# Performance work log

Measured on AMD Instinct MI355X. Metric: run time of the kernel, lower is better.

Reference implementation:

```python
import jax, jax.numpy as jnp
import numpy as np

B, T, S, L = 1, 2048, 512, 1024
C, H, Hk, D = 2048, 16, 4, 128
THETA = 10000.0


def setup_inputs() -> dict:
    key = jax.random.key(0)
    ks = jax.random.split(key, 9)
    sd = 0.02
    return {
        "x": jax.random.normal(ks[0], (B, T, C), jnp.float32),
        "stm": jax.random.normal(ks[1], (B, S, C), jnp.float32),
        "long_q": jax.random.normal(ks[2], (B, L, H, D), jnp.float32),
        "long_k": jax.random.normal(ks[3], (B, L, Hk, D), jnp.float32),
        "long_v": jax.random.normal(ks[4], (B, L, Hk, D), jnp.float32),
        "Wq": jax.random.normal(ks[5], (C, C), jnp.float32) * sd,
        "Wk": jax.random.normal(ks[6], (C, Hk * D), jnp.float32) * sd,
        "Wv": jax.random.normal(ks[7], (C, Hk * D), jnp.float32) * sd,
        "Wo": jax.random.normal(ks[8], (C, C), jnp.float32) * sd,
    }


def _rope_cos_sin(n, d, theta):
    # precompute_freqs_cis: freqs over even dims, angles t*freq
    freqs = 1.0 / (theta ** (jnp.arange(0, d, 2, dtype=jnp.float32) / d))
    ang = jnp.arange(n, dtype=jnp.float32)[:, None] * freqs[None, :]  # (n, d/2)
    return jnp.cos(ang), jnp.sin(ang)


def _apply_rope(x, cos, sin):
    # x: (B, n, h, D); complex-pair rotation over consecutive dims
    x1, x2 = x[..., 0::2], x[..., 1::2]
    c = cos[None, :, None, :]
    s = sin[None, :, None, :]
    r1 = x1 * c - x2 * s
    r2 = x1 * s + x2 * c
    return jnp.stack([r1, r2], axis=-1).reshape(x.shape)


def reference(x, stm, long_q, long_k, long_v, Wq, Wk, Wv, Wo):
    Bb, Tt, Cc = x.shape
    Ss, Ll = stm.shape[1], long_q.shape[1]
    seq = jnp.concatenate([stm, x], axis=1)  # (B, S+T, C)
    q = jnp.concatenate([long_q, (seq @ Wq).reshape(Bb, Ss + Tt, H, D)], axis=1)
    k = jnp.concatenate([long_k, (seq @ Wk).reshape(Bb, Ss + Tt, Hk, D)], axis=1)
    v = jnp.concatenate([long_v, (seq @ Wv).reshape(Bb, Ss + Tt, Hk, D)], axis=1)
    # inline RoPE on the last T+S positions only (memory bank keeps fixed encoding)
    cos, sin = _rope_cos_sin(Ss + Tt, D, THETA)
    q = q.at[:, Ll:].set(_apply_rope(q[:, Ll:], cos, sin))
    k = k.at[:, Ll:].set(_apply_rope(k[:, Ll:], cos, sin))
    tot = Ll + Ss + Tt
    # structured memory mask: causal over full stream, memory keys (< L+S) visible to all
    idx = jnp.arange(tot)
    mask = (idx[None, :] <= idx[:, None]) | (idx[None, :] < Ll + Ss)  # (tot, tot)
    # GQA: repeat_interleave kv heads
    rep = H // Hk
    kr = jnp.repeat(k, rep, axis=2)  # (B, tot, H, D)
    vr = jnp.repeat(v, rep, axis=2)
    att = jnp.einsum("bihd,bjhd->bhij", q, kr) * (1.0 / np.sqrt(D))
    att = jnp.where(mask[None, None], att, -jnp.inf)
    att = jax.nn.softmax(att, axis=-1)
    y = jnp.einsum("bhij,bjhd->bihd", att, vr).reshape(Bb, tot, Cc)
    y = y[:, -Tt:]  # keep only current-block outputs
    return y @ Wo
```

## Files before the change

### kernel.cpp

```cpp
#include <hip/hip_runtime.h>
#include <hip/hip_bf16.h>

typedef __attribute__((ext_vector_type(8))) short short8;
typedef __attribute__((ext_vector_type(4))) short short4v;
typedef __attribute__((ext_vector_type(4))) float f32x4;
typedef __attribute__((ext_vector_type(4))) float float4v;
typedef __attribute__((ext_vector_type(4))) int i32x4;

#define DEVFN static __device__ __forceinline__

#define T_N   2048
#define S_N   512
#define L_N   1024
#define C_N   2048
#define H_N   16
#define HK_N  4
#define D_N   128
#define ST_N  2560
#define TOT_N 3584
#define KV_N  512

DEVFN short f2bf(float f) {
  union { float f; unsigned u; } v; v.f = f;
  return (short)((v.u + 0x7FFFu + ((v.u >> 16) & 1u)) >> 16);
}
DEVFN float bf2f(short s) {
  union { unsigned u; float f; } v; v.u = ((unsigned)(unsigned short)s) << 16;
  return v.f;
}
DEVFN void gload16(const void* g, void* l) {
  __builtin_amdgcn_global_load_lds(
      (__attribute__((address_space(1))) void*)(g),
      (__attribute__((address_space(3))) void*)(l), 16, 0, 0);
}

#define Q_A (S_N * C_N / 4)
#define Q_B (Q_A + T_N * C_N / 4)
#define Q_C (Q_B + L_N * KV_N / 4)
#define Q_D (Q_C + L_N * KV_N / 4)
#define TAB_E (Q_D + ST_N * 64)
__global__ void k_setup(const float* __restrict__ x, const float* __restrict__ stm,
                        const float* __restrict__ lk, const float* __restrict__ lv,
                        short* __restrict__ seq, short* __restrict__ Kf,
                        short* __restrict__ Vf, float* __restrict__ ct,
                        float* __restrict__ st_) {
  int i = blockIdx.x * 256 + threadIdx.x;
  if (i < Q_D) {
    const float* src; short* dst; int off;
    if (i < Q_A)      { src = stm; dst = seq;                         off = i; }
    else if (i < Q_B) { src = x;   dst = seq + (size_t)S_N * C_N;     off = i - Q_A; }
    else if (i < Q_C) { src = lk;  dst = Kf;                          off = i - Q_B; }
    else              { src = lv;  dst = Vf;                          off = i - Q_C; }
    float4v v = reinterpret_cast<const float4v*>(src)[off];
    short4v o;
    o[0] = f2bf(v[0]); o[1] = f2bf(v[1]); o[2] = f2bf(v[2]); o[3] = f2bf(v[3]);
    reinterpret_cast<short4v*>(dst)[off] = o;
  } else {
    int j = i - Q_D;
    int p = j >> 6, fq = j & 63;
    float freq = expf(-(float)fq * (logf(10000.0f) / 64.0f));
    float ang = (float)p * freq;
    ct[j] = cosf(ang);
    st_[j] = sinf(ang);
  }
}

__global__ void k_tconv_all(const float* __restrict__ Wq, const float* __restrict__ Wk,
                            const float* __restrict__ Wv, const float* __restrict__ Wo,
                            short* __restrict__ WqT, short* __restrict__ WkT,
                            short* __restrict__ WvT, short* __restrict__ WoT) {
  __shared__ float tile[32][33];
  const int z = blockIdx.z;
  const float* in = (z == 0) ? Wq : (z == 1) ? Wk : (z == 2) ? Wv : Wo;
  short* outp     = (z == 0) ? WqT : (z == 1) ? WkT : (z == 2) ? WvT : WoT;
  const int cols = (z == 1 || z == 2) ? KV_N : C_N;
  if (blockIdx.x * 32 >= cols) return;
  int c0 = blockIdx.x * 32, r0 = blockIdx.y * 32;
  int tx = threadIdx.x, ty = threadIdx.y;
#pragma unroll
  for (int i = 0; i < 4; i++)
    tile[ty + i * 8][tx] = in[(size_t)(r0 + ty + i * 8) * cols + c0 + tx];
  __syncthreads();
#pragma unroll
  for (int i = 0; i < 4; i++)
    outp[(size_t)(c0 + ty + i * 8) * C_N + r0 + tx] = f2bf(tile[tx][ty + i * 8]);
}

__global__ void k_tv(const short* __restrict__ vf, short* __restrict__ vt) {
  __shared__ short tile[32][33];
  int hk = blockIdx.z;
  int r0 = blockIdx.x * 32;
  int d0 = blockIdx.y * 32;
  int tx = threadIdx.x, ty = threadIdx.y;
#pragma unroll
  for (int i = 0; i < 4; i++)
    tile[ty + i * 8][tx] = vf[(size_t)(r0 + ty + i * 8) * KV_N + hk * D_N + d0 + tx];
  __syncthreads();
  short* o = vt + (size_t)hk * D_N * TOT_N;
#pragma unroll
  for (int i = 0; i < 4; i++)
    o[(size_t)(d0 + ty + i * 8) * TOT_N + r0 + tx] = tile[tx][ty + i * 8];
}

__global__ __launch_bounds__(256) void k_gemm_o(
    const short* __restrict__ A, const short* __restrict__ Bt,
    float* __restrict__ C) {
  __shared__ short lbuf[2 * 6144];
  const int tid = threadIdx.x;
  const int w = tid >> 6, l = tid & 63;
  const int l15 = l & 15, lh = l >> 4;
  const int f0 = blockIdx.x;
  const int f = ((f0 & 7) << 6) + (f0 >> 3);
  const int rb = (f >> 4) << 6, cb = (f & 15) << 7;
  const int wr = (w >> 1) << 5, wc = (w & 1) << 6;
  f32x4 acc[2][4] = {};
  const int cA = tid;
  const short* pa = &A[(size_t)(rb + (cA >> 2)) * 2048 + (((cA ^ (cA >> 2)) & 3) << 3)];
  const int cB0 = tid, cB1 = 256 + tid;
  const short* pb0 = &Bt[(size_t)(cb + (cB0 >> 2)) * 2048 + (((cB0 ^ (cB0 >> 2)) & 3) << 3)];
  const short* pb1 = &Bt[(size_t)(cb + (cB1 >> 2)) * 2048 + (((cB1 ^ (cB1 >> 2)) & 3) << 3)];
  const int offA  = (w * 64) << 4;
  const int offB0 = 4096 + ((w * 64) << 4);
  const int offB1 = 4096 + ((256 + w * 64) << 4);
  char* lbase = (char*)lbuf;
  const int sw = (lh ^ (l15 & 3)) << 3;
  gload16(pa,  lbase + offA);
  gload16(pb0, lbase + offB0);
  gload16(pb1, lbase + offB1);
  int cur = 0;
  for (int kt = 0; kt < 2048; kt += 32) {
    const bool more = (kt + 32 < 2048);
    if (more) {
      char* p = lbase + (cur ^ 1) * 12288;
      gload16(pa  + kt + 32, p + offA);
      gload16(pb0 + kt + 32, p + offB0);
      gload16(pb1 + kt + 32, p + offB1);
      asm volatile("s_waitcnt vmcnt(3)" ::: "memory");
    } else {
      asm volatile("s_waitcnt vmcnt(0)" ::: "memory");
    }
    __builtin_amdgcn_s_barrier();
    __builtin_amdgcn_sched_barrier(0);
    const short* la = (const short*)(lbase + cur * 12288);
    const short* lb = (const short*)(lbase + cur * 12288 + 4096);
    short8 af[2], bg[4];
#pragma unroll
    for (int m = 0; m < 2; m++)
      af[m] = *reinterpret_cast<const short8*>(&la[(wr + m * 16 + l15) * 32 + sw]);
#pragma unroll
    for (int n = 0; n < 4; n++)
      bg[n] = *reinterpret_cast<const short8*>(&lb[(wc + n * 16 + l15) * 32 + sw]);
    __builtin_amdgcn_s_setprio(1);
#pragma unroll
    for (int m = 0; m < 2; m++)
#pragma unroll
      for (int n = 0; n < 4; n++)
        acc[m][n] = __builtin_amdgcn_mfma_f32_16x16x32_bf16(af[m], bg[n], acc[m][n], 0, 0, 0);
    __builtin_amdgcn_s_setprio(0);
    asm volatile("s_waitcnt lgkmcnt(0)" ::: "memory");
    __builtin_amdgcn_sched_barrier(0);
    __builtin_amdgcn_s_barrier();
    __builtin_amdgcn_sched_barrier(0);
    cur ^= 1;
  }
#pragma unroll
  for (int m = 0; m < 2; m++)
#pragma unroll
    for (int n = 0; n < 4; n++)
#pragma unroll
      for (int r = 0; r < 4; r++) {
        int row = rb + wr + m * 16 + lh * 4 + r;
        int col = cb + wc + n * 16 + l15;
        C[(size_t)row * 2048 + col] = acc[m][n][r];
      }
}

__global__ __launch_bounds__(256) void k_gemm_qkv(
    const short* __restrict__ A, const short* __restrict__ Bt,
    short* __restrict__ qbuf, short* __restrict__ Kf, short* __restrict__ Vf,
    const float* __restrict__ ct, const float* __restrict__ st_) {
  __shared__ short lbuf[2 * 6144];
  const int tid = threadIdx.x;
  const int w = tid >> 6, l = tid & 63;
  const int l15 = l & 15, lh = l >> 4;
  const int f0 = blockIdx.x;
  const int f = (f0 % 8) * 104 + f0 / 8;
  int rb, cb;
  if (f < 512) {
    cb = (f & 15) << 7;
    rb = 512 + ((f >> 4) << 6);
  } else {
    int g = f - 512;
    cb = (16 + (g & 7)) << 7;
    rb = (g >> 3) << 6;
  }
  const int wr = (w >> 1) << 5, wc = (w & 1) << 6;
  f32x4 acc[2][4] = {};
  const int cA = tid;
  const short* pa = &A[(size_t)(rb + (cA >> 2)) * 2048 + (((cA ^ (cA >> 2)) & 3) << 3)];
  const int cB0 = tid, cB1 = 256 + tid;
  const short* pb0 = &Bt[(size_t)(cb + (cB0 >> 2)) * 2048 + (((cB0 ^ (cB0 >> 2)) & 3) << 3)];
  const short* pb1 = &Bt[(size_t)(cb + (cB1 >> 2)) * 2048 + (((cB1 ^ (cB1 >> 2)) & 3) << 3)];
  const int offA  = (w * 64) << 4;
  const int offB0 = 4096 + ((w * 64) << 4);
  const int offB1 = 4096 + ((256 + w * 64) << 4);
  char* lbase = (char*)lbuf;
  const int sw = (lh ^ (l15 & 3)) << 3;
  gload16(pa,  lbase + offA);
  gload16(pb0, lbase + offB0);
  gload16(pb1, lbase + offB1);
  int cur = 0;
  for (int kt = 0; kt < 2048; kt += 32) {
    const bool more = (kt + 32 < 2048);
    if (more) {
      char* p = lbase + (cur ^ 1) * 12288;
      gload16(pa  + kt + 32, p + offA);
      gload16(pb0 + kt + 32, p + offB0);
      gload16(pb1 + kt + 32, p + offB1);
      asm volatile("s_waitcnt vmcnt(3)" ::: "memory");
    } else {
      asm volatile("s_waitcnt vmcnt(0)" ::: "memory");
    }
    __builtin_amdgcn_s_barrier();
    __builtin_amdgcn_sched_barrier(0);
    const short* la = (const short*)(lbase + cur * 12288);
    const short* lb = (const short*)(lbase + cur * 12288 + 4096);
    short8 af[2], bg[4];
#pragma unroll
    for (int m = 0; m < 2; m++)
      af[m] = *reinterpret_cast<const short8*>(&la[(wr + m * 16 + l15) * 32 + sw]);
#pragma unroll
    for (int n = 0; n < 4; n++)
      bg[n] = *reinterpret_cast<const short8*>(&lb[(wc + n * 16 + l15) * 32 + sw]);
    __builtin_amdgcn_s_setprio(1);
#pragma unroll
    for (int m = 0; m < 2; m++)
#pragma unroll
      for (int n = 0; n < 4; n++)
        acc[m][n] = __builtin_amdgcn_mfma_f32_16x16x32_bf16(af[m], bg[n], acc[m][n], 0, 0, 0);
    __builtin_amdgcn_s_setprio(0);
    asm volatile("s_waitcnt lgkmcnt(0)" ::: "memory");
    __builtin_amdgcn_sched_barrier(0);
    __builtin_amdgcn_s_barrier();
    __builtin_amdgcn_sched_barrier(0);
    cur ^= 1;
  }
#pragma unroll
  for (int m = 0; m < 2; m++)
#pragma unroll
    for (int n = 0; n < 4; n++) {
      int coln = cb + wc + n * 16 + l15;
      const bool do_rope = coln < 2560;
      const int fidx = (coln & 127) >> 1;
#pragma unroll
      for (int r = 0; r < 4; r++) {
        int row = rb + wr + m * 16 + lh * 4 + r;
        float v = acc[m][n][r];
        float other = __shfl_xor(v, 1, 64);
        if (do_rope) {
          float co = ct[row * 64 + fidx];
          float si = st_[row * 64 + fidx];
          v = (l15 & 1) ? (other * si + v * co) : (v * co - other * si);
        }
        short bv = f2bf(v);
        if (coln < 2048) {
          if (row >= 512) qbuf[(size_t)(row - 512) * C_N + coln] = bv;
        } else if (coln < 2560) {
          Kf[(size_t)(L_N + row) * KV_N + (coln - 2048)] = bv;
        } else {
          Vf[(size_t)(L_N + row) * KV_N + (coln - 2560)] = bv;
        }
      }
    }
}

__global__ __launch_bounds__(256, 4) void k_attn(
    const short* __restrict__ Q,
    const short* __restrict__ Kf,
    const short* __restrict__ Vt,
    short* __restrict__ pY,
    float* __restrict__ pM,
    float* __restrict__ pL) {
  __shared__ short kl[64 * 128];
  __shared__ short vl[128 * 64];
  const int f = blockIdx.x;
  const int p = f >> 9;
  const int f5 = f & 511;
  const int hk = f5 & 3;
  const int qraw = (f5 >> 2) & 31;
  const int hh = (f5 >> 7) & 3;
  const int qb = (f5 & 256) ? (31 - qraw) : qraw;
  const int h = hk * 4 + hh;
  const int tid = threadIdx.x, w = tid >> 6, l = tid & 63;
  const int l15 = l & 15, lh = l >> 4;
  const int qbase = qb << 6;
  const int qrow0 = qbase + (w << 4);
  short8 aq[4];
#pragma unroll
  for (int kb = 0; kb < 4; kb++)
    aq[kb] = *reinterpret_cast<const short8*>(
        &Q[(size_t)(qrow0 + l15) * C_N + h * D_N + kb * 32 + lh * 8]);
  short8 ones;
#pragma unroll
  for (int j = 0; j < 8; j++) ones[j] = (short)0x3F80;
  f32x4 yacc[8] = {};
  f32x4 lacc = {};
  float m_r = -3.0e38f;
  const float K2 = 0.12751744f;
  const float THR = 90.0f;
  const int nkt = (1663 + qbase) >> 6;
  const int th = nkt >> 1;
  const int t0 = p ? th : 0;
  const int t1 = p ? nkt : th;
  const short* psk[4];
  const short* psv[4];
  int ldsoff[4];
#pragma unroll
  for (int it = 0; it < 4; it++) {
    int c = it * 256 + tid;
    int kr = c >> 4, kkc = c & 15;
    int pkr = (kr & 0x23) | ((kr & 0x0C) << 1) | ((kr >> 2) & 4);
    psk[it] = &Kf[(size_t)pkr * KV_N + hk * D_N + ((kkc ^ (kr & 7)) << 3)];
    int vrow = c >> 3, vkc = c & 7;
    psv[it] = &Vt[(size_t)hk * D_N * TOT_N + (size_t)vrow * TOT_N + ((vkc ^ (vrow & 7)) << 3)];
    ldsoff[it] = (it * 256 + w * 64) << 4;
  }
#pragma unroll
  for (int it = 0; it < 4; it++)
    gload16(psk[it] + (size_t)t0 * 64 * KV_N, (char*)kl + ldsoff[it]);
#pragma unroll
  for (int it = 0; it < 4; it++)
    gload16(psv[it] + (size_t)t0 * 64, (char*)vl + ldsoff[it]);
  __syncthreads();
  for (int t = t0; t < t1; t++) {
    const bool more = (t + 1 < t1);
    short8 kreg[4], vreg[4];
    if (more) {
#pragma unroll
      for (int it = 0; it < 4; it++)
        kreg[it] = *reinterpret_cast<const short8*>(psk[it] + (size_t)(t + 1) * 64 * KV_N);
#pragma unroll
      for (int it = 0; it < 4; it++)
        vreg[it] = *reinterpret_cast<const short8*>(psv[it] + (size_t)(t + 1) * 64);
    }
    f32x4 s[4] = {};
    __builtin_amdgcn_s_setprio(1);
#pragma unroll
    for (int g = 0; g < 4; g++) {
      int row = g * 16 + l15;
#pragma unroll
      for (int kb = 0; kb < 4; kb++) {
        short8 bk = *reinterpret_cast<const short8*>(
            (const char*)kl + row * 256 + ((((kb << 2) + lh) ^ (row & 7)) << 4));
        s[g] = __builtin_amdgcn_mfma_f32_16x16x32_bf16(bk, aq[kb], s[g], 0, 0, 0);
      }
    }
    __builtin_amdgcn_s_setprio(0);
    if ((t * 64 + 63) > (1536 + qrow0)) {
      int qi = qrow0 + l15;
#pragma unroll
      for (int g = 0; g < 4; g++)
#pragma unroll
        for (int r = 0; r < 4; r++) {
          int key = t * 64 + ((g >> 1) << 5) + (lh << 3) + ((g & 1) << 2) + r;
          if (key > 1536 + qi) s[g][r] = -3.0e38f;
        }
    }
    float lm = s[0][0];
#pragma unroll
    for (int g = 0; g < 4; g++)
#pragma unroll
      for (int r = 0; r < 4; r++) lm = fmaxf(lm, s[g][r]);
    if (!__all(lm <= m_r + THR)) {
      float rm = fmaxf(lm, __shfl_xor(lm, 16, 64));
      rm = fmaxf(rm, __shfl_xor(rm, 32, 64));
      float mn = fmaxf(m_r, rm);
      float scf = __builtin_amdgcn_exp2f((m_r - mn) * K2);
      m_r = mn;
#pragma unroll
      for (int r = 0; r < 4; r++) {
        float sc_c = __shfl(scf, lh * 4 + r, 64);
        lacc[r] *= sc_c;
#pragma unroll
        for (int dg = 0; dg < 8; dg++) yacc[dg][r] *= sc_c;
      }
    }
    const float mk = m_r * K2;
    float pvv[16];
#pragma unroll
    for (int g = 0; g < 4; g++)
#pragma unroll
      for (int r = 0; r < 4; r++)
        pvv[g * 4 + r] = __builtin_amdgcn_exp2f(s[g][r] * K2 - mk);
    union { i32x4 wv; short8 sv; } u0, u1;
#pragma unroll
    for (int j = 0; j < 4; j++) {
      unsigned w0, w1;
      int g0 = (j >> 1), b0 = g0 * 4 + 2 * (j & 1);
      int g1 = 2 + (j >> 1), b1 = g1 * 4 + 2 * (j & 1);
      asm("v_cvt_pk_bf16_f32 %0, %1, %2" : "=v"(w0) : "v"(pvv[b0]), "v"(pvv[b0 + 1]));
      asm("v_cvt_pk_bf16_f32 %0, %1, %2" : "=v"(w1) : "v"(pvv[b1]), "v"(pvv[b1 + 1]));
      u0.wv[j] = (int)w0;
      u1.wv[j] = (int)w1;
    }
    lacc = __builtin_amdgcn_mfma_f32_16x16x32_bf16(u0.sv, ones, lacc, 0, 0, 0);
    lacc = __builtin_amdgcn_mfma_f32_16x16x32_bf16(u1.sv, ones, lacc, 0, 0, 0);
    __builtin_amdgcn_s_setprio(1);
#pragma unroll
    for (int dg = 0; dg < 8; dg++) {
      int vrow = dg * 16 + l15;
      short8 bv0 = *reinterpret_cast<const short8*>(
          (const char*)vl + (vrow << 7) + ((lh ^ (vrow & 7)) << 4));
      yacc[dg] = __builtin_amdgcn_mfma_f32_16x16x32_bf16(u0.sv, bv0, yacc[dg], 0, 0, 0);
      short8 bv1 = *reinterpret_cast<const short8*>(
          (const char*)vl + (vrow << 7) + (((4 + lh) ^ (vrow & 7)) << 4));
      yacc[dg] = __builtin_amdgcn_mfma_f32_16x16x32_bf16(u1.sv, bv1, yacc[dg], 0, 0, 0);
    }
    __builtin_amdgcn_s_setprio(0);
    asm volatile("s_waitcnt lgkmcnt(0)" ::: "memory");
    __builtin_amdgcn_sched_barrier(0);
    __builtin_amdgcn_s_barrier();
    __builtin_amdgcn_sched_barrier(0);
    if (more) {
#pragma unroll
      for (int it = 0; it < 4; it++)
        *reinterpret_cast<short8*>((char*)kl + ldsoff[it] + (l << 4)) = kreg[it];
#pragma unroll
      for (int it = 0; it < 4; it++)
        *reinterpret_cast<short8*>((char*)vl + ldsoff[it] + (l << 4)) = vreg[it];
    }
    __syncthreads();
  }
  const size_t base = (size_t)(p * 16 + h) * 2048;
#pragma unroll
  for (int dg = 0; dg < 8; dg++)
#pragma unroll
    for (int r = 0; r < 4; r++) {
      int row = qrow0 + lh * 4 + r;
      pY[(base + row) * 128 + dg * 16 + l15] = f2bf(yacc[dg][r]);
    }
#pragma unroll
  for (int r = 0; r < 4; r++)
    if (l15 == 0) pL[base + qrow0 + lh * 4 + r] = lacc[r];
  if (lh == 0) pM[base + qrow0 + l15] = m_r;
}

__global__ void k_merge(const short* __restrict__ pY, const float* __restrict__ pM,
                        const float* __restrict__ pL, short* __restrict__ Y) {
  const int h = blockIdx.y;
  const int row = blockIdx.x * 16 + (threadIdx.x >> 4);
  const int d0 = (threadIdx.x & 15) * 8;
  const size_t b0 = (size_t)h * 2048 + row;
  const size_t b1 = (size_t)(16 + h) * 2048 + row;
  const float K2 = 0.12751744f;
  float m0 = pM[b0], m1 = pM[b1];
  float l0 = pL[b0], l1 = pL[b1];
  float M = fmaxf(m0, m1);
  float a0 = __builtin_amdgcn_exp2f((m0 - M) * K2);
  float a1 = __builtin_amdgcn_exp2f((m1 - M) * K2);
  float inv = 1.0f / (l0 * a0 + l1 * a1);
  short8 y0 = *reinterpret_cast<const short8*>(&pY[b0 * 128 + d0]);
  short8 y1 = *reinterpret_cast<const short8*>(&pY[b1 * 128 + d0]);
  short8 o;
#pragma unroll
  for (int j = 0; j < 8; j++)
    o[j] = f2bf((bf2f(y0[j]) * a0 + bf2f(y1[j]) * a1) * inv);
  *reinterpret_cast<short8*>(&Y[(size_t)row * C_N + h * D_N + d0]) = o;
}

extern "C" void kernel_launch(void* const* d_in, const int* in_sizes, int n_in,
                              void* d_out, int out_size, void* d_ws, size_t ws_size,
                              hipStream_t stream) {
  const float* x      = (const float*)d_in[0];
  const float* stm    = (const float*)d_in[1];
  const float* long_k = (const float*)d_in[3];
  const float* long_v = (const float*)d_in[4];
  const float* Wq     = (const float*)d_in[5];
  const float* Wk     = (const float*)d_in[6];
  const float* Wv     = (const float*)d_in[7];
  const float* Wo     = (const float*)d_in[8];
  float* out = (float*)d_out;

  short* seq  = (short*)d_ws;
  short* WqT  = seq  + (size_t)ST_N * C_N;
  short* WkT  = WqT  + (size_t)C_N * C_N;
  short* WvT  = WkT  + (size_t)KV_N * C_N;
  short* WoT  = WvT  + (size_t)KV_N * C_N;
  short* qbuf = WoT  + (size_t)C_N * C_N;
  short* Kf   = qbuf + (size_t)T_N * C_N;
  short* Vf   = Kf   + (size_t)TOT_N * KV_N;
  short* Vt   = Vf   + (size_t)TOT_N * KV_N;
  short* ybuf = Vt   + (size_t)TOT_N * KV_N;
  float* ctab = (float*)(ybuf + (size_t)T_N * C_N);
  float* stab = ctab + (size_t)ST_N * 64;

  short* pY = (short*)d_ws;
  float* pM = (float*)(pY + (size_t)2 * 16 * 2048 * 128);
  float* pL = pM + (size_t)2 * 16 * 2048;

  k_setup<<<TAB_E / 256, 256, 0, stream>>>(x, stm, long_k, long_v, seq, Kf, Vf, ctab, stab);

  k_tconv_all<<<dim3(64, 64, 4), dim3(32, 8), 0, stream>>>(
      Wq, Wk, Wv, Wo, WqT, WkT, WvT, WoT);

  k_gemm_qkv<<<832, 256, 0, stream>>>(seq, WqT, qbuf, Kf, Vf, ctab, stab);

  k_tv<<<dim3(TOT_N / 32, D_N / 32, HK_N), dim3(32, 8), 0, stream>>>(Vf, Vt);

  k_attn<<<1024, 256, 0, stream>>>(qbuf, Kf, Vt, pY, pM, pL);

  k_merge<<<dim3(128, 16), 256, 0, stream>>>(pY, pM, pL, ybuf);

  k_gemm_o<<<512, 256, 0, stream>>>(ybuf, WoT, out);
}
```

Measured before the change: 200.3 us.

## Process two 16-row query tiles per wave in attention to reuse K/V LDS loads

Each wave now handles 32 query rows (two 16-row sub-tiles A and B) instead of 16, so every K and V fragment read from LDS feeds two MFMAs and each block's K/V tile loads are amortized over 128 query rows. The grid halves to 512 blocks and launch bounds drop to 2 waves per SIMD to make room for the doubled accumulators. The causal key-tile count is recomputed for the larger query block and masking is applied per sub-tile. The cost is higher register pressure, lower occupancy and fewer blocks to spread the causal-imbalanced work across CUs.

```diff
diff --git a/kernel.cpp b/kernel.cpp
--- a/kernel.cpp
+++ b/kernel.cpp
@@ -274,7 +274,7 @@
     }
 }
 
-__global__ __launch_bounds__(256, 4) void k_attn(
+__global__ __launch_bounds__(256, 2) void k_attn(
     const short* __restrict__ Q,
     const short* __restrict__ Kf,
     const short* __restrict__ Vt,
@@ -284,31 +284,34 @@
   __shared__ short kl[64 * 128];
   __shared__ short vl[128 * 64];
   const int f = blockIdx.x;
-  const int p = f >> 9;
-  const int f5 = f & 511;
-  const int hk = f5 & 3;
-  const int qraw = (f5 >> 2) & 31;
-  const int hh = (f5 >> 7) & 3;
-  const int qb = (f5 & 256) ? (31 - qraw) : qraw;
+  const int p = f >> 8;
+  const int f8 = f & 255;
+  const int hk = f8 & 3;
+  const int qraw = (f8 >> 2) & 15;
+  const int hh = (f8 >> 6) & 3;
+  const int qb = p ? (15 - qraw) : qraw;
   const int h = hk * 4 + hh;
   const int tid = threadIdx.x, w = tid >> 6, l = tid & 63;
   const int l15 = l & 15, lh = l >> 4;
-  const int qbase = qb << 6;
-  const int qrow0 = qbase + (w << 4);
-  short8 aq[4];
-#pragma unroll
-  for (int kb = 0; kb < 4; kb++)
-    aq[kb] = *reinterpret_cast<const short8*>(
+  const int qbase = qb << 7;
+  const int qrow0 = qbase + (w << 5);
+  short8 aqA[4], aqB[4];
+#pragma unroll
+  for (int kb = 0; kb < 4; kb++) {
+    aqA[kb] = *reinterpret_cast<const short8*>(
         &Q[(size_t)(qrow0 + l15) * C_N + h * D_N + kb * 32 + lh * 8]);
+    aqB[kb] = *reinterpret_cast<const short8*>(
+        &Q[(size_t)(qrow0 + 16 + l15) * C_N + h * D_N + kb * 32 + lh * 8]);
+  }
   short8 ones;
 #pragma unroll
   for (int j = 0; j < 8; j++) ones[j] = (short)0x3F80;
-  f32x4 yacc[8] = {};
-  f32x4 lacc = {};
-  float m_r = -3.0e38f;
+  f32x4 yA[8] = {}, yB[8] = {};
+  f32x4 lA_ = {}, lB_ = {};
+  float mA = -3.0e38f, mB = -3.0e38f;
   const float K2 = 0.12751744f;
   const float THR = 90.0f;
-  const int nkt = (1663 + qbase) >> 6;
+  const int nkt = ((qbase + 1663) >> 6) + 1;
   const int th = nkt >> 1;
   const int t0 = p ? th : 0;
   const int t1 = p ? nkt : th;
@@ -343,7 +346,7 @@
       for (int it = 0; it < 4; it++)
         vreg[it] = *reinterpret_cast<const short8*>(psv[it] + (size_t)(t + 1) * 64);
     }
-    f32x4 s[4] = {};
+    f32x4 sA[4] = {}, sB[4] = {};
     __builtin_amdgcn_s_setprio(1);
 #pragma unroll
     for (int g = 0; g < 4; g++) {
@@ -352,7 +355,8 @@
       for (int kb = 0; kb < 4; kb++) {
         short8 bk = *reinterpret_cast<const short8*>(
             (const char*)kl + row * 256 + ((((kb << 2) + lh) ^ (row & 7)) << 4));
-        s[g] = __builtin_amdgcn_mfma_f32_16x16x32_bf16(bk, aq[kb], s[g], 0, 0, 0);
+        sA[g] = __builtin_amdgcn_mfma_f32_16x16x32_bf16(bk, aqA[kb], sA[g], 0, 0, 0);
+        sB[g] = __builtin_amdgcn_mfma_f32_16x16x32_bf16(bk, aqB[kb], sB[g], 0, 0, 0);
       }
     }
     __builtin_amdgcn_s_setprio(0);
@@ -363,58 +367,116 @@
 #pragma unroll
         for (int r = 0; r < 4; r++) {
           int key = t * 64 + ((g >> 1) << 5) + (lh << 3) + ((g & 1) << 2) + r;
-          if (key > 1536 + qi) s[g][r] = -3.0e38f;
+          if (key > 1536 + qi) sA[g][r] = -3.0e38f;
         }
     }
-    float lm = s[0][0];
-#pragma unroll
-    for (int g = 0; g < 4; g++)
-#pragma unroll
-      for (int r = 0; r < 4; r++) lm = fmaxf(lm, s[g][r]);
-    if (!__all(lm <= m_r + THR)) {
-      float rm = fmaxf(lm, __shfl_xor(lm, 16, 64));
-      rm = fmaxf(rm, __shfl_xor(rm, 32, 64));
-      float mn = fmaxf(m_r, rm);
-      float scf = __builtin_amdgcn_exp2f((m_r - mn) * K2);
-      m_r = mn;
-#pragma unroll
-      for (int r = 0; r < 4; r++) {
-        float sc_c = __shfl(scf, lh * 4 + r, 64);
-        lacc[r] *= sc_c;
-#pragma unroll
-        for (int dg = 0; dg < 8; dg++) yacc[dg][r] *= sc_c;
-      }
-    }
-    const float mk = m_r * K2;
-    float pvv[16];
-#pragma unroll
-    for (int g = 0; g < 4; g++)
-#pragma unroll
-      for (int r = 0; r < 4; r++)
-        pvv[g * 4 + r] = __builtin_amdgcn_exp2f(s[g][r] * K2 - mk);
-    union { i32x4 wv; short8 sv; } u0, u1;
-#pragma unroll
-    for (int j = 0; j < 4; j++) {
-      unsigned w0, w1;
-      int g0 = (j >> 1), b0 = g0 * 4 + 2 * (j & 1);
-      int g1 = 2 + (j >> 1), b1 = g1 * 4 + 2 * (j & 1);
-      asm("v_cvt_pk_bf16_f32 %0, %1, %2" : "=v"(w0) : "v"(pvv[b0]), "v"(pvv[b0 + 1]));
-      asm("v_cvt_pk_bf16_f32 %0, %1, %2" : "=v"(w1) : "v"(pvv[b1]), "v"(pvv[b1 + 1]));
-      u0.wv[j] = (int)w0;
-      u1.wv[j] = (int)w1;
-    }
-    lacc = __builtin_amdgcn_mfma_f32_16x16x32_bf16(u0.sv, ones, lacc, 0, 0, 0);
-    lacc = __builtin_amdgcn_mfma_f32_16x16x32_bf16(u1.sv, ones, lacc, 0, 0, 0);
+    if ((t * 64 + 63) > (1536 + qrow0 + 16)) {
+      int qi = qrow0 + 16 + l15;
+#pragma unroll
+      for (int g = 0; g < 4; g++)
+#pragma unroll
+        for (int r = 0; r < 4; r++) {
+          int key = t * 64 + ((g >> 1) << 5) + (lh << 3) + ((g & 1) << 2) + r;
+          if (key > 1536 + qi) sB[g][r] = -3.0e38f;
+        }
+    }
+    {
+      float lm = sA[0][0];
+#pragma unroll
+      for (int g = 0; g < 4; g++)
+#pragma unroll
+        for (int r = 0; r < 4; r++) lm = fmaxf(lm, sA[g][r]);
+      if (!__all(lm <= mA + THR)) {
+        float rm = fmaxf(lm, __shfl_xor(lm, 16, 64));
+        rm = fmaxf(rm, __shfl_xor(rm, 32, 64));
+        float mn = fmaxf(mA, rm);
+        float scf = __builtin_amdgcn_exp2f((mA - mn) * K2);
+        mA = mn;
+#pragma unroll
+        for (int r = 0; r < 4; r++) {
+          float sc_c = __shfl(scf, lh * 4 + r, 64);
+          lA_[r] *= sc_c;
+#pragma unroll
+          for (int dg = 0; dg < 8; dg++) yA[dg][r] *= sc_c;
+        }
+      }
+    }
+    {
+      float lm = sB[0][0];
+#pragma unroll
+      for (int g = 0; g < 4; g++)
+#pragma unroll
+        for (int r = 0; r < 4; r++) lm = fmaxf(lm, sB[g][r]);
+      if (!__all(lm <= mB + THR)) {
+        float rm = fmaxf(lm, __shfl_xor(lm, 16, 64));
+        rm = fmaxf(rm, __shfl_xor(rm, 32, 64));
+        float mn = fmaxf(mB, rm);
+        float scf = __builtin_amdgcn_exp2f((mB - mn) * K2);
+        mB = mn;
+#pragma unroll
+        for (int r = 0; r < 4; r++) {
+          float sc_c = __shfl(scf, lh * 4 + r, 64);
+          lB_[r] *= sc_c;
+#pragma unroll
+          for (int dg = 0; dg < 8; dg++) yB[dg][r] *= sc_c;
+        }
+      }
+    }
+    union { i32x4 wv; short8 sv; } uA0, uA1, uB0, uB1;
+    {
+      const float mk = mA * K2;
+      float pvv[16];
+#pragma unroll
+      for (int g = 0; g < 4; g++)
+#pragma unroll
+        for (int r = 0; r < 4; r++)
+          pvv[g * 4 + r] = __builtin_amdgcn_exp2f(sA[g][r] * K2 - mk);
+#pragma unroll
+      for (int j = 0; j < 4; j++) {
+        unsigned w0, w1;
+        int b0 = (j >> 1) * 4 + 2 * (j & 1);
+        int b1 = (2 + (j >> 1)) * 4 + 2 * (j & 1);
+        asm("v_cvt_pk_bf16_f32 %0, %1, %2" : "=v"(w0) : "v"(pvv[b0]), "v"(pvv[b0 + 1]));
+        asm("v_cvt_pk_bf16_f32 %0, %1, %2" : "=v"(w1) : "v"(pvv[b1]), "v"(pvv[b1 + 1]));
+        uA0.wv[j] = (int)w0;
+        uA1.wv[j] = (int)w1;
+      }
+    }
+    {
+      const float mk = mB * K2;
+      float pvv[16];
+#pragma unroll
+      for (int g = 0; g < 4; g++)
+#pragma unroll
+        for (int r = 0; r < 4; r++)
+          pvv[g * 4 + r] = __builtin_amdgcn_exp2f(sB[g][r] * K2 - mk);
+#pragma unroll
+      for (int j = 0; j < 4; j++) {
+        unsigned w0, w1;
+        int b0 = (j >> 1) * 4 + 2 * (j & 1);
+        int b1 = (2 + (j >> 1)) * 4 + 2 * (j & 1);
+        asm("v_cvt_pk_bf16_f32 %0, %1, %2" : "=v"(w0) : "v"(pvv[b0]), "v"(pvv[b0 + 1]));
+        asm("v_cvt_pk_bf16_f32 %0, %1, %2" : "=v"(w1) : "v"(pvv[b1]), "v"(pvv[b1 + 1]));
+        uB0.wv[j] = (int)w0;
+        uB1.wv[j] = (int)w1;
+      }
+    }
+    lA_ = __builtin_amdgcn_mfma_f32_16x16x32_bf16(uA0.sv, ones, lA_, 0, 0, 0);
+    lA_ = __builtin_amdgcn_mfma_f32_16x16x32_bf16(uA1.sv, ones, lA_, 0, 0, 0);
+    lB_ = __builtin_amdgcn_mfma_f32_16x16x32_bf16(uB0.sv, ones, lB_, 0, 0, 0);
+    lB_ = __builtin_amdgcn_mfma_f32_16x16x32_bf16(uB1.sv, ones, lB_, 0, 0, 0);
     __builtin_amdgcn_s_setprio(1);
 #pragma unroll
     for (int dg = 0; dg < 8; dg++) {
       int vrow = dg * 16 + l15;
       short8 bv0 = *reinterpret_cast<const short8*>(
           (const char*)vl + (vrow << 7) + ((lh ^ (vrow & 7)) << 4));
-      yacc[dg] = __builtin_amdgcn_mfma_f32_16x16x32_bf16(u0.sv, bv0, yacc[dg], 0, 0, 0);
       short8 bv1 = *reinterpret_cast<const short8*>(
           (const char*)vl + (vrow << 7) + (((4 + lh) ^ (vrow & 7)) << 4));
-      yacc[dg] = __builtin_amdgcn_mfma_f32_16x16x32_bf16(u1.sv, bv1, yacc[dg], 0, 0, 0);
+      yA[dg] = __builtin_amdgcn_mfma_f32_16x16x32_bf16(uA0.sv, bv0, yA[dg], 0, 0, 0);
+      yA[dg] = __builtin_amdgcn_mfma_f32_16x16x32_bf16(uA1.sv, bv1, yA[dg], 0, 0, 0);
+      yB[dg] = __builtin_amdgcn_mfma_f32_16x16x32_bf16(uB0.sv, bv0, yB[dg], 0, 0, 0);
+      yB[dg] = __builtin_amdgcn_mfma_f32_16x16x32_bf16(uB1.sv, bv1, yB[dg], 0, 0, 0);
     }
     __builtin_amdgcn_s_setprio(0);
     asm volatile("s_waitcnt lgkmcnt(0)" ::: "memory");
@@ -436,13 +498,21 @@
   for (int dg = 0; dg < 8; dg++)
 #pragma unroll
     for (int r = 0; r < 4; r++) {
-      int row = qrow0 + lh * 4 + r;
-      pY[(base + row) * 128 + dg * 16 + l15] = f2bf(yacc[dg][r]);
-    }
-#pragma unroll
-  for (int r = 0; r < 4; r++)
-    if (l15 == 0) pL[base + qrow0 + lh * 4 + r] = lacc[r];
-  if (lh == 0) pM[base + qrow0 + l15] = m_r;
+      int rowA = qrow0 + lh * 4 + r;
+      pY[(base + rowA) * 128 + dg * 16 + l15] = f2bf(yA[dg][r]);
+      pY[(base + rowA + 16) * 128 + dg * 16 + l15] = f2bf(yB[dg][r]);
+    }
+  if (l15 == 0) {
+#pragma unroll
+    for (int r = 0; r < 4; r++) {
+      pL[base + qrow0 + lh * 4 + r] = lA_[r];
+      pL[base + qrow0 + 16 + lh * 4 + r] = lB_[r];
+    }
+  }
+  if (lh == 0) {
+    pM[base + qrow0 + l15] = mA;
+    pM[base + qrow0 + 16 + l15] = mB;
+  }
 }
 
 __global__ void k_merge(const short* __restrict__ pY, const float* __restrict__ pM,
@@ -507,7 +577,7 @@
 
   k_tv<<<dim3(TOT_N / 32, D_N / 32, HK_N), dim3(32, 8), 0, stream>>>(Vf, Vt);
 
-  k_attn<<<1024, 256, 0, stream>>>(qbuf, Kf, Vt, pY, pM, pL);
+  k_attn<<<512, 256, 0, stream>>>(qbuf, Kf, Vt, pY, pM, pL);
 
   k_merge<<<dim3(128, 16), 256, 0, stream>>>(pY, pM, pL, ybuf);
 
```

New measurement: 176.9 us. -11.7%, faster.
